# Kernel tuning notes

Hardware: AMD Instinct MI355X
Metric: run time of the kernel (lower is better)

The kernel has to match this reference:

```python
import jax, jax.numpy as jnp
import numpy as np

N_HEAD, D_MODEL, D_HEAD = 16, 1024, 64
QLEN, BSZ = 1024, 8
LN_EPS = 1e-5


def _rel_shift(x):
    # x: [b, n, i, j]; Transformer-XL relative shift via pad/reshape/slice
    b, n, i, j = x.shape
    x = jnp.pad(x, ((0, 0), (0, 0), (0, 0), (1, 0)))  # [b,n,i,j+1]
    x = x.reshape(b, n, j + 1, i)[:, :, 1:, :].reshape(b, n, i, j)
    return x


def setup_inputs() -> dict:
    key = jax.random.key(0)
    k = jax.random.split(key, 8)
    w = jax.random.normal(k[0], (QLEN, BSZ, D_MODEL), dtype=jnp.float32)
    r_emb = jax.random.normal(k[1], (QLEN, N_HEAD, D_HEAD), dtype=jnp.float32) * 0.02
    r_w_bias = jax.random.normal(k[2], (N_HEAD, D_HEAD), dtype=jnp.float32) * 0.02
    r_bias = jax.random.normal(k[3], (QLEN, N_HEAD), dtype=jnp.float32) * 0.02
    # causal mask: True means masked (j > i)
    attn_mask = jnp.triu(jnp.ones((QLEN, QLEN), dtype=bool), k=1)
    qkv_w = jax.random.normal(k[4], (D_MODEL, 3 * N_HEAD * D_HEAD), dtype=jnp.float32) * (D_MODEL ** -0.5)
    o_w = jax.random.normal(k[5], (N_HEAD * D_HEAD, D_MODEL), dtype=jnp.float32) * ((N_HEAD * D_HEAD) ** -0.5)
    ln_g = jnp.ones((D_MODEL,), dtype=jnp.float32)
    ln_b = jnp.zeros((D_MODEL,), dtype=jnp.float32)
    return {"w": w, "r_emb": r_emb, "r_w_bias": r_w_bias, "r_bias": r_bias,
            "qkv_w": qkv_w, "o_w": o_w, "ln_g": ln_g, "ln_b": ln_b,
            "attn_mask": attn_mask}


def reference(w, r_emb, r_w_bias, r_bias, qkv_w, o_w, ln_g, ln_b, attn_mask):
    qlen, bsz, d_model = w.shape
    n_head, d_head = r_w_bias.shape
    scale = 1.0 / (d_head ** 0.5)

    heads = w @ qkv_w  # [q, b, 3*H*D]
    q_h, k_h, v_h = jnp.split(heads, 3, axis=-1)
    q_h = q_h.reshape(qlen, bsz, n_head, d_head)
    k_h = k_h.reshape(qlen, bsz, n_head, d_head)
    v_h = v_h.reshape(qlen, bsz, n_head, d_head)

    # klen == qlen (no mems), r_emb/r_bias already length klen
    rw_q = q_h + r_w_bias[None, None]                      # [i,b,n,d]
    AC = jnp.einsum('ibnd,jbnd->bnij', rw_q, k_h)          # content score
    B_ = jnp.einsum('ibnd,jnd->bnij', q_h, r_emb)          # position score
    D_ = r_bias.T[None, :, None, :]                        # [1,n,1,j]
    BD = _rel_shift(B_ + D_)
    attn_score = scale * (AC + BD)                         # [b,n,i,j]

    attn_score = jnp.where(attn_mask[None, None], -jnp.inf, attn_score)
    attn_prob = jax.nn.softmax(attn_score, axis=3)

    attn_vec = jnp.einsum('bnij,jbnd->ibnd', attn_prob, v_h)
    attn_vec = attn_vec.reshape(qlen, bsz, n_head * d_head)
    attn_out = attn_vec @ o_w

    # post-LN residual
    y = w + attn_out
    mu = jnp.mean(y, axis=-1, keepdims=True)
    var = jnp.mean((y - mu) ** 2, axis=-1, keepdims=True)
    out = (y - mu) * jax.lax.rsqrt(var + LN_EPS) * ln_g + ln_b
    return out
```

## Files before the change

### kernel.cpp

```cpp
#include <hip/hip_runtime.h>

typedef unsigned short u16;
typedef __attribute__((ext_vector_type(8))) short bf16x8;
typedef __attribute__((ext_vector_type(4))) short bf16x4;
typedef __attribute__((ext_vector_type(4))) float f32x4;
typedef __attribute__((ext_vector_type(4))) unsigned short u16x4;

#define SEQ 1024
#define BSZ 8
#define NHD 16
#define DHD 64
#define DMODEL 1024

__device__ __forceinline__ u16 f2bf(float x) {
  unsigned u = __float_as_uint(x);
  return (u16)((u + 0x7fffu + ((u >> 16) & 1u)) >> 16);
}
__device__ __forceinline__ float bf2f(u16 h) {
  return __uint_as_float(((unsigned)h) << 16);
}

typedef const __attribute__((address_space(1))) unsigned int gu32_t;
typedef __attribute__((address_space(3))) unsigned int lu32_t;
__device__ __forceinline__ void gload16(const void* g, void* l) {
  __builtin_amdgcn_global_load_lds((gu32_t*)g, (lu32_t*)l, 16, 0, 0);
}

__global__ void cast_w_k(const float* __restrict__ in, u16* __restrict__ out) {
  size_t i = ((size_t)blockIdx.x * 256 + threadIdx.x) * 4;
  float4 v = *(const float4*)(in + i);
  u16x4 o;
  o[0] = f2bf(v.x); o[1] = f2bf(v.y); o[2] = f2bf(v.z); o[3] = f2bf(v.w);
  *(u16x4*)(out + i) = o;
}

__global__ void transpose_cast_k(const float* __restrict__ in, u16* __restrict__ out,
                                 int R, int C) {
  __shared__ float tile[32][33];
  int tx = threadIdx.x & 31, ty = threadIdx.x >> 5;
  int bx = blockIdx.x * 32, by = blockIdx.y * 32;
#pragma unroll
  for (int rr = ty; rr < 32; rr += 8)
    tile[rr][tx] = in[(size_t)(by + rr) * C + bx + tx];
  __syncthreads();
#pragma unroll
  for (int rr = ty; rr < 32; rr += 8)
    out[(size_t)(bx + rr) * R + by + tx] = f2bf(tile[tx][rr]);
}

__global__ void cast_remb_k(const float* __restrict__ in, u16* __restrict__ out) {
  int t0 = blockIdx.x * 256 + threadIdx.x;
  int jn = t0 >> 3, db = t0 & 7;
  int j = jn >> 4, n = jn & 15;
  const float* src = in + (size_t)jn * 64 + db * 8;
  u16* dst = out + (size_t)n * 65536 + (size_t)(j >> 4) * 1024 + (db >> 2) * 512 +
             (((j & 15) | ((db & 3) << 4)) << 3);
#pragma unroll
  for (int e = 0; e < 8; ++e) dst[e] = f2bf(src[e]);
}

__global__ void cvec_k(const float* __restrict__ remb, const float* __restrict__ rwb,
                       float* __restrict__ cv) {
  int idx = blockIdx.x * 256 + threadIdx.x;
  int n = idx >> 10, t = idx & 1023;
  const float* src = remb + (size_t)(t * 16 + n) * 64;
  const float* wb = rwb + n * 64;
  float s = 0.f;
#pragma unroll
  for (int d = 0; d < 64; ++d) s += src[d] * wb[d];
  cv[idx] = s;
}

template <int EPI>
__global__ __launch_bounds__(256) void gemm_bt(
    const u16* __restrict__ A, const u16* __restrict__ Bt, int K,
    u16* __restrict__ q_o, u16* __restrict__ k_o, u16* __restrict__ v_o,
    const float* __restrict__ resid, float* __restrict__ yout) {
  __shared__ __attribute__((aligned(16))) u16 ldsA[2][4096];
  __shared__ __attribute__((aligned(16))) u16 ldsB[2][4096];
  const int tid = threadIdx.x;
  const int wid = tid >> 6, l = tid & 63;
  const int l15 = l & 15, lg = l >> 4;
  const int bm = blockIdx.y, bn = blockIdx.x;
  const int wm = wid & 1, wn = wid >> 1;
  const size_t ldb = (size_t)K * 2;

  const char* aA = (const char*)A + (size_t)(bm * 128 + wid * 32 + (l >> 2)) * ldb + (l & 3) * 16;
  const char* aB = (const char*)Bt + (size_t)(bn * 128 + wid * 32 + (l >> 2)) * ldb + (l & 3) * 16;

  auto stage = [&](int buf, int kt) {
    const char* sa = aA + (size_t)kt * 64;
    const char* sb = aB + (size_t)kt * 64;
    char* la = (char*)&ldsA[buf][wid * 1024];
    char* lb = (char*)&ldsB[buf][wid * 1024];
    gload16(sa, la);
    gload16(sa + 16 * ldb, la + 1024);
    gload16(sb, lb);
    gload16(sb + 16 * ldb, lb + 1024);
  };

  f32x4 acc[4][4] = {};
  stage(0, 0);
  __syncthreads();
  const int NT = K >> 5;
  for (int t = 0; t < NT; ++t) {
    int cur = t & 1;
    if (t + 1 < NT) stage(cur ^ 1, t + 1);
    bf16x8 af[4], bfr[4];
#pragma unroll
    for (int mi = 0; mi < 4; ++mi)
      af[mi] = *(const bf16x8*)&ldsA[cur][(wm * 64 + mi * 16 + l15) * 32 + lg * 8];
#pragma unroll
    for (int ni = 0; ni < 4; ++ni)
      bfr[ni] = *(const bf16x8*)&ldsB[cur][(wn * 64 + ni * 16 + l15) * 32 + lg * 8];
#pragma unroll
    for (int mi = 0; mi < 4; ++mi)
#pragma unroll
      for (int ni = 0; ni < 4; ++ni)
        acc[mi][ni] = __builtin_amdgcn_mfma_f32_16x16x32_bf16(af[mi], bfr[ni], acc[mi][ni], 0, 0, 0);
    __syncthreads();
  }

  if (EPI == 0) {
#pragma unroll
    for (int mi = 0; mi < 4; ++mi)
#pragma unroll
      for (int ni = 0; ni < 4; ++ni) {
        int c = bn * 128 + wn * 64 + ni * 16 + l15;
        int which = c >> 10, rem = c & 1023, h = rem >> 6, d = rem & 63;
        u16* dst = which == 0 ? q_o : (which == 1 ? k_o : v_o);
#pragma unroll
        for (int r = 0; r < 4; ++r) {
          int rg = bm * 128 + wm * 64 + mi * 16 + lg * 4 + r;
          int i = rg >> 3, bb = rg & 7;
          int bn2 = bb * 16 + h;
          size_t idx;
          if (which == 0) {
            idx = ((size_t)bn2 * 1024 + i) * 64 + d;
          } else if (which == 1) {
            idx = (size_t)bn2 * 65536 + (size_t)(i >> 4) * 1024 + (d >> 5) * 512 +
                  (((i & 15) | (((d >> 3) & 3) << 4)) << 3) + (d & 7);
          } else {
            idx = (size_t)bn2 * 65536 + (size_t)(i >> 4) * 1024 + (d >> 4) * 256 +
                  (((d & 15) | (((i >> 2) & 3) << 4)) << 2) + (i & 3);
          }
          dst[idx] = f2bf(acc[mi][ni][r]);
        }
      }
  } else {
#pragma unroll
    for (int mi = 0; mi < 4; ++mi)
#pragma unroll
      for (int ni = 0; ni < 4; ++ni) {
        int c = bn * 128 + wn * 64 + ni * 16 + l15;
#pragma unroll
        for (int r = 0; r < 4; ++r) {
          int rg = bm * 128 + wm * 64 + mi * 16 + lg * 4 + r;
          size_t off = (size_t)rg * 1024 + c;
          yout[off] = resid[off] + acc[mi][ni][r];
        }
      }
  }
}

__global__ __launch_bounds__(256, 4) void attn_k(
    const u16* __restrict__ qg, const u16* __restrict__ kf, const u16* __restrict__ vf,
    const u16* __restrict__ rf, const float* __restrict__ rbias,
    const float* __restrict__ cvec, const float* __restrict__ rwb,
    u16* __restrict__ av) {
  __shared__ __attribute__((aligned(16))) float Elds[4][16][84];
  __shared__ __attribute__((aligned(16))) float rb[1088];

  const int tid = threadIdx.x;
  const int wid = tid >> 6, l = tid & 63;
  const int l15 = l & 15, lg = l >> 4;
  const int id = blockIdx.x;
  const int qblk = 15 - (id >> 7);
  const int n = (id & 7) | (((id >> 3) & 1) << 3);
  const int b = (id >> 4) & 7;
  const int bn = b * 16 + n;
  const int ib = qblk * 64;
  const int iw = ib + wid * 16;

  for (int idx = tid; idx < 1088; idx += 256)
    rb[idx] = (idx < 1024) ? (rbias[idx * 16 + n] - cvec[n * 1024 + idx]) : 0.f;

  const u16* qrow = qg + ((size_t)bn * 1024 + iw + l15) * 64;
  const float* wbp = rwb + n * 64;
  bf16x8 qr0 = *(const bf16x8*)(qrow + lg * 8);
  bf16x8 qr1 = *(const bf16x8*)(qrow + 32 + lg * 8);
  bf16x8 qw0, qw1;
#pragma unroll
  for (int e = 0; e < 8; ++e) {
    qw0[e] = (short)f2bf(bf2f((u16)qr0[e]) + wbp[lg * 8 + e]);
    qw1[e] = (short)f2bf(bf2f((u16)qr1[e]) + wbp[32 + lg * 8 + e]);
  }

  f32x4 oacc[4] = {};
  float m_run = -1e30f, l_run = 0.f;

  const u16* kfp = kf + (size_t)bn * 65536 + l * 8;
  const u16* vfp = vf + (size_t)bn * 65536 + l * 4;
  const u16* rfp = rf + (size_t)n * 65536 + l * 8;

  __syncthreads();

  const int njt = qblk + 1;
  for (int jt = 0; jt < njt; ++jt) {
    const int jb = jt * 64;

    const u16* kt = kfp + jt * 4096;
    bf16x8 kf00 = *(const bf16x8*)(kt);
    bf16x8 kf01 = *(const bf16x8*)(kt + 512);
    bf16x8 kf10 = *(const bf16x8*)(kt + 1024);
    bf16x8 kf11 = *(const bf16x8*)(kt + 1536);
    bf16x8 kf20 = *(const bf16x8*)(kt + 2048);
    bf16x8 kf21 = *(const bf16x8*)(kt + 2560);
    bf16x8 kf30 = *(const bf16x8*)(kt + 3072);
    bf16x8 kf31 = *(const bf16x8*)(kt + 3584);

    const int tb = jb - iw + 1008;
    const int tb16 = tb >> 4;
#pragma unroll
    for (int f = 0; f < 5; ++f) {
      int t16 = tb16 + f;
      if (t16 > 63) t16 = 63;
      const u16* rr = rfp + t16 * 1024;
      bf16x8 ra0 = *(const bf16x8*)(rr);
      bf16x8 ra1 = *(const bf16x8*)(rr + 512);
      f32x4 et = {};
      et = __builtin_amdgcn_mfma_f32_16x16x32_bf16(ra0, qw0, et, 0, 0, 0);
      et = __builtin_amdgcn_mfma_f32_16x16x32_bf16(ra1, qw1, et, 0, 0, 0);
      f32x4 rb4 = *(const f32x4*)&rb[tb + f * 16 + lg * 4];
      et = et + rb4;
      *(f32x4*)&Elds[wid][l15][f * 16 + lg * 4] = et;
    }

    f32x4 st[4];
    __builtin_amdgcn_s_setprio(1);
    {
      f32x4 a;
      a = __builtin_amdgcn_mfma_f32_16x16x32_bf16(kf00, qw0, (f32x4){}, 0, 0, 0);
      st[0] = __builtin_amdgcn_mfma_f32_16x16x32_bf16(kf01, qw1, a, 0, 0, 0);
      a = __builtin_amdgcn_mfma_f32_16x16x32_bf16(kf10, qw0, (f32x4){}, 0, 0, 0);
      st[1] = __builtin_amdgcn_mfma_f32_16x16x32_bf16(kf11, qw1, a, 0, 0, 0);
      a = __builtin_amdgcn_mfma_f32_16x16x32_bf16(kf20, qw0, (f32x4){}, 0, 0, 0);
      st[2] = __builtin_amdgcn_mfma_f32_16x16x32_bf16(kf21, qw1, a, 0, 0, 0);
      a = __builtin_amdgcn_mfma_f32_16x16x32_bf16(kf30, qw0, (f32x4){}, 0, 0, 0);
      st[3] = __builtin_amdgcn_mfma_f32_16x16x32_bf16(kf31, qw1, a, 0, 0, 0);
    }
    __builtin_amdgcn_s_setprio(0);

    const u16* vt0 = vfp + jt * 4096;
    bf16x4 va0 = *(const bf16x4*)(vt0);
    bf16x4 va1 = *(const bf16x4*)(vt0 + 1024);
    bf16x4 va2 = *(const bf16x4*)(vt0 + 2048);
    bf16x4 va3 = *(const bf16x4*)(vt0 + 3072);

    const bool domask = (jb == ib);
    float tmax = -1e30f;
#pragma unroll
    for (int jj = 0; jj < 4; ++jj)
#pragma unroll
      for (int r2 = 0; r2 < 4; ++r2) {
        int jl = jj * 16 + lg * 4 + r2;
        float v = st[jj][r2] + Elds[wid][l15][jl - l15 + 15];
        v *= 0.125f;
        if (domask && (jl > wid * 16 + l15)) v = -1e30f;
        st[jj][r2] = v;
        tmax = fmaxf(tmax, v);
      }
    tmax = fmaxf(tmax, __shfl_xor(tmax, 16));
    tmax = fmaxf(tmax, __shfl_xor(tmax, 32));

    if (!__all(tmax - m_run <= 8.0f)) {
      float m_new = fmaxf(m_run, tmax);
      float fac = __expf(m_run - m_new);
      m_run = m_new;
      l_run *= fac;
      float fo[4];
#pragma unroll
      for (int r2 = 0; r2 < 4; ++r2) fo[r2] = __shfl(fac, (l & 48) | (lg * 4 + r2));
#pragma unroll
      for (int dd = 0; dd < 4; ++dd)
#pragma unroll
        for (int r2 = 0; r2 < 4; ++r2) oacc[dd][r2] *= fo[r2];
    }

    float psum = 0.f;
    bf16x4 pa[4];
#pragma unroll
    for (int jj = 0; jj < 4; ++jj)
#pragma unroll
      for (int r2 = 0; r2 < 4; ++r2) {
        float p = __expf(st[jj][r2] - m_run);
        psum += p;
        pa[jj][r2] = (short)f2bf(p);
      }
    psum += __shfl_xor(psum, 16);
    psum += __shfl_xor(psum, 32);
    l_run += psum;

    __builtin_amdgcn_s_setprio(1);
    {
      const u16* vt1 = vt0 + 256;
      bf16x4 vb0 = *(const bf16x4*)(vt1);
      bf16x4 vb1 = *(const bf16x4*)(vt1 + 1024);
      bf16x4 vb2 = *(const bf16x4*)(vt1 + 2048);
      bf16x4 vb3 = *(const bf16x4*)(vt1 + 3072);
      oacc[0] = __builtin_amdgcn_mfma_f32_16x16x16bf16_1k(pa[0], va0, oacc[0], 0, 0, 0);
      oacc[0] = __builtin_amdgcn_mfma_f32_16x16x16bf16_1k(pa[1], va1, oacc[0], 0, 0, 0);
      oacc[0] = __builtin_amdgcn_mfma_f32_16x16x16bf16_1k(pa[2], va2, oacc[0], 0, 0, 0);
      oacc[0] = __builtin_amdgcn_mfma_f32_16x16x16bf16_1k(pa[3], va3, oacc[0], 0, 0, 0);
      const u16* vt2 = vt0 + 512;
      va0 = *(const bf16x4*)(vt2);
      va1 = *(const bf16x4*)(vt2 + 1024);
      va2 = *(const bf16x4*)(vt2 + 2048);
      va3 = *(const bf16x4*)(vt2 + 3072);
      oacc[1] = __builtin_amdgcn_mfma_f32_16x16x16bf16_1k(pa[0], vb0, oacc[1], 0, 0, 0);
      oacc[1] = __builtin_amdgcn_mfma_f32_16x16x16bf16_1k(pa[1], vb1, oacc[1], 0, 0, 0);
      oacc[1] = __builtin_amdgcn_mfma_f32_16x16x16bf16_1k(pa[2], vb2, oacc[1], 0, 0, 0);
      oacc[1] = __builtin_amdgcn_mfma_f32_16x16x16bf16_1k(pa[3], vb3, oacc[1], 0, 0, 0);
      const u16* vt3 = vt0 + 768;
      vb0 = *(const bf16x4*)(vt3);
      vb1 = *(const bf16x4*)(vt3 + 1024);
      vb2 = *(const bf16x4*)(vt3 + 2048);
      vb3 = *(const bf16x4*)(vt3 + 3072);
      oacc[2] = __builtin_amdgcn_mfma_f32_16x16x16bf16_1k(pa[0], va0, oacc[2], 0, 0, 0);
      oacc[2] = __builtin_amdgcn_mfma_f32_16x16x16bf16_1k(pa[1], va1, oacc[2], 0, 0, 0);
      oacc[2] = __builtin_amdgcn_mfma_f32_16x16x16bf16_1k(pa[2], va2, oacc[2], 0, 0, 0);
      oacc[2] = __builtin_amdgcn_mfma_f32_16x16x16bf16_1k(pa[3], va3, oacc[2], 0, 0, 0);
      oacc[3] = __builtin_amdgcn_mfma_f32_16x16x16bf16_1k(pa[0], vb0, oacc[3], 0, 0, 0);
      oacc[3] = __builtin_amdgcn_mfma_f32_16x16x16bf16_1k(pa[1], vb1, oacc[3], 0, 0, 0);
      oacc[3] = __builtin_amdgcn_mfma_f32_16x16x16bf16_1k(pa[2], vb2, oacc[3], 0, 0, 0);
      oacc[3] = __builtin_amdgcn_mfma_f32_16x16x16bf16_1k(pa[3], vb3, oacc[3], 0, 0, 0);
    }
    __builtin_amdgcn_s_setprio(0);
  }

  float linv = 1.f / l_run;
  float io[4];
#pragma unroll
  for (int r2 = 0; r2 < 4; ++r2) io[r2] = __shfl(linv, (l & 48) | (lg * 4 + r2));
#pragma unroll
  for (int dd = 0; dd < 4; ++dd)
#pragma unroll
    for (int r2 = 0; r2 < 4; ++r2) {
      int ig = iw + lg * 4 + r2;
      av[((size_t)ig * 8 + b) * 1024 + n * 64 + dd * 16 + l15] = f2bf(oacc[dd][r2] * io[r2]);
    }
}

__global__ void ln_k(float* __restrict__ y, const float* __restrict__ g,
                     const float* __restrict__ be) {
  const int row = blockIdx.x, tid = threadIdx.x;
  float* p = y + (size_t)row * 1024;
  float4 v = ((const float4*)p)[tid];
  float s1 = v.x + v.y + v.z + v.w;
  float s2 = v.x * v.x + v.y * v.y + v.z * v.z + v.w * v.w;
#pragma unroll
  for (int mk = 1; mk < 64; mk <<= 1) {
    s1 += __shfl_xor(s1, mk);
    s2 += __shfl_xor(s2, mk);
  }
  __shared__ float as1[4], as2[4];
  if ((tid & 63) == 0) { as1[tid >> 6] = s1; as2[tid >> 6] = s2; }
  __syncthreads();
  s1 = as1[0] + as1[1] + as1[2] + as1[3];
  s2 = as2[0] + as2[1] + as2[2] + as2[3];
  float mu = s1 * (1.f / 1024.f);
  float var = s2 * (1.f / 1024.f) - mu * mu;
  float rs = rsqrtf(var + 1e-5f);
  float4 gg = ((const float4*)g)[tid];
  float4 bb = ((const float4*)be)[tid];
  float4 o;
  o.x = (v.x - mu) * rs * gg.x + bb.x;
  o.y = (v.y - mu) * rs * gg.y + bb.y;
  o.z = (v.z - mu) * rs * gg.z + bb.z;
  o.w = (v.w - mu) * rs * gg.w + bb.w;
  ((float4*)p)[tid] = o;
}

extern "C" void kernel_launch(void* const* d_in, const int* in_sizes, int n_in,
                              void* d_out, int out_size, void* d_ws, size_t ws_size,
                              hipStream_t stream) {
  (void)in_sizes; (void)n_in; (void)out_size; (void)ws_size;
  const float* w      = (const float*)d_in[0];
  const float* r_emb  = (const float*)d_in[1];
  const float* r_wb   = (const float*)d_in[2];
  const float* r_bias = (const float*)d_in[3];
  const float* qkv_w  = (const float*)d_in[4];
  const float* o_w    = (const float*)d_in[5];
  const float* ln_g   = (const float*)d_in[6];
  const float* ln_b   = (const float*)d_in[7];
  float* out = (float*)d_out;
  char* ws = (char*)d_ws;

  u16* w_b    = (u16*)(ws + 0);
  u16* qkvw_t = (u16*)(ws + 16777216);
  u16* ow_t   = (u16*)(ws + 23068672);
  u16* remb_f = (u16*)(ws + 25165824);
  u16* q_b    = (u16*)(ws + 27262976);
  u16* k_f    = (u16*)(ws + 44040192);
  u16* v_f    = (u16*)(ws + 60817408);
  float* cvb  = (float*)(ws + 77594624);
  u16* av_b   = w_b;

  cast_w_k<<<8192, 256, 0, stream>>>(w, w_b);
  transpose_cast_k<<<dim3(96, 32), 256, 0, stream>>>(qkv_w, qkvw_t, 1024, 3072);
  transpose_cast_k<<<dim3(32, 32), 256, 0, stream>>>(o_w, ow_t, 1024, 1024);
  cast_remb_k<<<512, 256, 0, stream>>>(r_emb, remb_f);
  cvec_k<<<64, 256, 0, stream>>>(r_emb, r_wb, cvb);
  gemm_bt<0><<<dim3(24, 64), 256, 0, stream>>>(w_b, qkvw_t, 1024, q_b, k_f, v_f, nullptr, nullptr);
  attn_k<<<dim3(2048), 256, 0, stream>>>(q_b, k_f, v_f, remb_f, r_bias, cvb, r_wb, av_b);
  gemm_bt<1><<<dim3(8, 64), 256, 0, stream>>>(av_b, ow_t, 1024, nullptr, nullptr, nullptr, w, out);
  ln_k<<<8192, 256, 0, stream>>>(out, ln_g, ln_b);
}
```

Baseline: 224.3 us.

## Process two 16-row query tiles per wave to reuse K/V/R fragment loads

Each wave in the attention kernel now handles 32 query rows (two 16-row tiles A and B) instead of 16, so every K, V and relative-embedding fragment loaded from global memory feeds twice as many MFMAs. The positional-score tile computation is shared across both tiles via six R fragments instead of five per tile, and the grid is halved to 1024 blocks with launch bounds lowered to 3 blocks per CU. This cuts redundant global/L2 traffic per unit of work, at the cost of higher register pressure, lower occupancy and coarser causal load balancing, since waves within a block now have different loop trip counts.

```diff
diff --git a/kernel.cpp b/kernel.cpp
--- a/kernel.cpp
+++ b/kernel.cpp
@@ -163,191 +163,202 @@
   }
 }
 
-__global__ __launch_bounds__(256, 4) void attn_k(
+__global__ __launch_bounds__(256, 3) void attn_k(
     const u16* __restrict__ qg, const u16* __restrict__ kf, const u16* __restrict__ vf,
     const u16* __restrict__ rf, const float* __restrict__ rbias,
     const float* __restrict__ cvec, const float* __restrict__ rwb,
     u16* __restrict__ av) {
-  __shared__ __attribute__((aligned(16))) float Elds[4][16][84];
+  __shared__ __attribute__((aligned(16))) float EldsA[4][16][84];
+  __shared__ __attribute__((aligned(16))) float EldsB[4][16][84];
   __shared__ __attribute__((aligned(16))) float rb[1088];
 
   const int tid = threadIdx.x;
   const int wid = tid >> 6, l = tid & 63;
   const int l15 = l & 15, lg = l >> 4;
   const int id = blockIdx.x;
-  const int qblk = 15 - (id >> 7);
+  const int qblk = 7 - (id >> 7);
   const int n = (id & 7) | (((id >> 3) & 1) << 3);
   const int b = (id >> 4) & 7;
   const int bn = b * 16 + n;
-  const int ib = qblk * 64;
-  const int iw = ib + wid * 16;
+  const int ib = qblk * 128;
+  const int iw = ib + wid * 32;
 
   for (int idx = tid; idx < 1088; idx += 256)
     rb[idx] = (idx < 1024) ? (rbias[idx * 16 + n] - cvec[n * 1024 + idx]) : 0.f;
 
-  const u16* qrow = qg + ((size_t)bn * 1024 + iw + l15) * 64;
   const float* wbp = rwb + n * 64;
-  bf16x8 qr0 = *(const bf16x8*)(qrow + lg * 8);
-  bf16x8 qr1 = *(const bf16x8*)(qrow + 32 + lg * 8);
-  bf16x8 qw0, qw1;
+  const u16* qrowA = qg + ((size_t)bn * 1024 + iw + l15) * 64;
+  const u16* qrowB = qrowA + 16 * 64;
+  bf16x8 qa0 = *(const bf16x8*)(qrowA + lg * 8);
+  bf16x8 qa1 = *(const bf16x8*)(qrowA + 32 + lg * 8);
+  bf16x8 qb0 = *(const bf16x8*)(qrowB + lg * 8);
+  bf16x8 qb1 = *(const bf16x8*)(qrowB + 32 + lg * 8);
+  bf16x8 qwA0, qwA1, qwB0, qwB1;
 #pragma unroll
   for (int e = 0; e < 8; ++e) {
-    qw0[e] = (short)f2bf(bf2f((u16)qr0[e]) + wbp[lg * 8 + e]);
-    qw1[e] = (short)f2bf(bf2f((u16)qr1[e]) + wbp[32 + lg * 8 + e]);
-  }
-
-  f32x4 oacc[4] = {};
-  float m_run = -1e30f, l_run = 0.f;
+    float w0 = wbp[lg * 8 + e], w1 = wbp[32 + lg * 8 + e];
+    qwA0[e] = (short)f2bf(bf2f((u16)qa0[e]) + w0);
+    qwA1[e] = (short)f2bf(bf2f((u16)qa1[e]) + w1);
+    qwB0[e] = (short)f2bf(bf2f((u16)qb0[e]) + w0);
+    qwB1[e] = (short)f2bf(bf2f((u16)qb1[e]) + w1);
+  }
+
+  f32x4 oaccA[4] = {}, oaccB[4] = {};
+  float mA = -1e30f, lA = 0.f, mB = -1e30f, lB = 0.f;
 
   const u16* kfp = kf + (size_t)bn * 65536 + l * 8;
   const u16* vfp = vf + (size_t)bn * 65536 + l * 4;
   const u16* rfp = rf + (size_t)n * 65536 + l * 8;
 
+  const int dAm = (iw & 63) + l15;
+  const int dBm = dAm + 16;
+
   __syncthreads();
 
-  const int njt = qblk + 1;
+  const int njt = (iw >> 6) + 1;
   for (int jt = 0; jt < njt; ++jt) {
     const int jb = jt * 64;
 
     const u16* kt = kfp + jt * 4096;
-    bf16x8 kf00 = *(const bf16x8*)(kt);
-    bf16x8 kf01 = *(const bf16x8*)(kt + 512);
-    bf16x8 kf10 = *(const bf16x8*)(kt + 1024);
-    bf16x8 kf11 = *(const bf16x8*)(kt + 1536);
-    bf16x8 kf20 = *(const bf16x8*)(kt + 2048);
-    bf16x8 kf21 = *(const bf16x8*)(kt + 2560);
-    bf16x8 kf30 = *(const bf16x8*)(kt + 3072);
-    bf16x8 kf31 = *(const bf16x8*)(kt + 3584);
-
-    const int tb = jb - iw + 1008;
-    const int tb16 = tb >> 4;
-#pragma unroll
-    for (int f = 0; f < 5; ++f) {
-      int t16 = tb16 + f;
+    bf16x8 kk[8];
+#pragma unroll
+    for (int s = 0; s < 8; ++s) kk[s] = *(const bf16x8*)(kt + s * 512);
+
+    const int tbB = jb - iw - 16 + 1008;
+    const int t16b = tbB >> 4;
+#pragma unroll
+    for (int f = 0; f < 6; ++f) {
+      int t16 = t16b + f;
       if (t16 > 63) t16 = 63;
       const u16* rr = rfp + t16 * 1024;
       bf16x8 ra0 = *(const bf16x8*)(rr);
       bf16x8 ra1 = *(const bf16x8*)(rr + 512);
-      f32x4 et = {};
-      et = __builtin_amdgcn_mfma_f32_16x16x32_bf16(ra0, qw0, et, 0, 0, 0);
-      et = __builtin_amdgcn_mfma_f32_16x16x32_bf16(ra1, qw1, et, 0, 0, 0);
-      f32x4 rb4 = *(const f32x4*)&rb[tb + f * 16 + lg * 4];
-      et = et + rb4;
-      *(f32x4*)&Elds[wid][l15][f * 16 + lg * 4] = et;
+      f32x4 rb4 = *(const f32x4*)&rb[tbB + f * 16 + lg * 4];
+      if (f < 5) {
+        f32x4 et = {};
+        et = __builtin_amdgcn_mfma_f32_16x16x32_bf16(ra0, qwB0, et, 0, 0, 0);
+        et = __builtin_amdgcn_mfma_f32_16x16x32_bf16(ra1, qwB1, et, 0, 0, 0);
+        *(f32x4*)&EldsB[wid][l15][f * 16 + lg * 4] = et + rb4;
+      }
+      if (f >= 1) {
+        f32x4 et = {};
+        et = __builtin_amdgcn_mfma_f32_16x16x32_bf16(ra0, qwA0, et, 0, 0, 0);
+        et = __builtin_amdgcn_mfma_f32_16x16x32_bf16(ra1, qwA1, et, 0, 0, 0);
+        *(f32x4*)&EldsA[wid][l15][(f - 1) * 16 + lg * 4] = et + rb4;
+      }
     }
 
-    f32x4 st[4];
+    f32x4 stA[4], stB[4];
     __builtin_amdgcn_s_setprio(1);
-    {
-      f32x4 a;
-      a = __builtin_amdgcn_mfma_f32_16x16x32_bf16(kf00, qw0, (f32x4){}, 0, 0, 0);
-      st[0] = __builtin_amdgcn_mfma_f32_16x16x32_bf16(kf01, qw1, a, 0, 0, 0);
-      a = __builtin_amdgcn_mfma_f32_16x16x32_bf16(kf10, qw0, (f32x4){}, 0, 0, 0);
-      st[1] = __builtin_amdgcn_mfma_f32_16x16x32_bf16(kf11, qw1, a, 0, 0, 0);
-      a = __builtin_amdgcn_mfma_f32_16x16x32_bf16(kf20, qw0, (f32x4){}, 0, 0, 0);
-      st[2] = __builtin_amdgcn_mfma_f32_16x16x32_bf16(kf21, qw1, a, 0, 0, 0);
-      a = __builtin_amdgcn_mfma_f32_16x16x32_bf16(kf30, qw0, (f32x4){}, 0, 0, 0);
-      st[3] = __builtin_amdgcn_mfma_f32_16x16x32_bf16(kf31, qw1, a, 0, 0, 0);
+#pragma unroll
+    for (int jj = 0; jj < 4; ++jj) {
+      f32x4 a = __builtin_amdgcn_mfma_f32_16x16x32_bf16(kk[jj * 2], qwA0, (f32x4){}, 0, 0, 0);
+      stA[jj] = __builtin_amdgcn_mfma_f32_16x16x32_bf16(kk[jj * 2 + 1], qwA1, a, 0, 0, 0);
+    }
+#pragma unroll
+    for (int jj = 0; jj < 4; ++jj) {
+      f32x4 a = __builtin_amdgcn_mfma_f32_16x16x32_bf16(kk[jj * 2], qwB0, (f32x4){}, 0, 0, 0);
+      stB[jj] = __builtin_amdgcn_mfma_f32_16x16x32_bf16(kk[jj * 2 + 1], qwB1, a, 0, 0, 0);
     }
     __builtin_amdgcn_s_setprio(0);
 
     const u16* vt0 = vfp + jt * 4096;
-    bf16x4 va0 = *(const bf16x4*)(vt0);
-    bf16x4 va1 = *(const bf16x4*)(vt0 + 1024);
-    bf16x4 va2 = *(const bf16x4*)(vt0 + 2048);
-    bf16x4 va3 = *(const bf16x4*)(vt0 + 3072);
-
-    const bool domask = (jb == ib);
-    float tmax = -1e30f;
+    bf16x4 vv[4][4];
+#pragma unroll
+    for (int jj = 0; jj < 4; ++jj)
+#pragma unroll
+      for (int dd = 0; dd < 4; ++dd)
+        vv[jj][dd] = *(const bf16x4*)(vt0 + jj * 1024 + dd * 256);
+
+    const bool domask = (jt == njt - 1);
+    float tmaxA = -1e30f, tmaxB = -1e30f;
 #pragma unroll
     for (int jj = 0; jj < 4; ++jj)
 #pragma unroll
       for (int r2 = 0; r2 < 4; ++r2) {
         int jl = jj * 16 + lg * 4 + r2;
-        float v = st[jj][r2] + Elds[wid][l15][jl - l15 + 15];
-        v *= 0.125f;
-        if (domask && (jl > wid * 16 + l15)) v = -1e30f;
-        st[jj][r2] = v;
-        tmax = fmaxf(tmax, v);
-      }
-    tmax = fmaxf(tmax, __shfl_xor(tmax, 16));
-    tmax = fmaxf(tmax, __shfl_xor(tmax, 32));
-
-    if (!__all(tmax - m_run <= 8.0f)) {
-      float m_new = fmaxf(m_run, tmax);
-      float fac = __expf(m_run - m_new);
-      m_run = m_new;
-      l_run *= fac;
-      float fo[4];
-#pragma unroll
-      for (int r2 = 0; r2 < 4; ++r2) fo[r2] = __shfl(fac, (l & 48) | (lg * 4 + r2));
+        float va = stA[jj][r2] + EldsA[wid][l15][jl - l15 + 15];
+        float vb = stB[jj][r2] + EldsB[wid][l15][jl - l15 + 15];
+        va *= 0.125f; vb *= 0.125f;
+        if (domask) {
+          if (jl > dAm) va = -1e30f;
+          if (jl > dBm) vb = -1e30f;
+        }
+        stA[jj][r2] = va; stB[jj][r2] = vb;
+        tmaxA = fmaxf(tmaxA, va); tmaxB = fmaxf(tmaxB, vb);
+      }
+    tmaxA = fmaxf(tmaxA, __shfl_xor(tmaxA, 16));
+    tmaxA = fmaxf(tmaxA, __shfl_xor(tmaxA, 32));
+    tmaxB = fmaxf(tmaxB, __shfl_xor(tmaxB, 16));
+    tmaxB = fmaxf(tmaxB, __shfl_xor(tmaxB, 32));
+
+    if (!__all(fmaxf(tmaxA - mA, tmaxB - mB) <= 8.0f)) {
+      float mnA = fmaxf(mA, tmaxA), mnB = fmaxf(mB, tmaxB);
+      float facA = __expf(mA - mnA), facB = __expf(mB - mnB);
+      mA = mnA; mB = mnB;
+      lA *= facA; lB *= facB;
+      float foA[4], foB[4];
+#pragma unroll
+      for (int r2 = 0; r2 < 4; ++r2) {
+        foA[r2] = __shfl(facA, (l & 48) | (lg * 4 + r2));
+        foB[r2] = __shfl(facB, (l & 48) | (lg * 4 + r2));
+      }
 #pragma unroll
       for (int dd = 0; dd < 4; ++dd)
 #pragma unroll
-        for (int r2 = 0; r2 < 4; ++r2) oacc[dd][r2] *= fo[r2];
+        for (int r2 = 0; r2 < 4; ++r2) {
+          oaccA[dd][r2] *= foA[r2];
+          oaccB[dd][r2] *= foB[r2];
+        }
     }
 
-    float psum = 0.f;
-    bf16x4 pa[4];
+    float psA = 0.f, psB = 0.f;
+    bf16x4 paA[4], paB[4];
 #pragma unroll
     for (int jj = 0; jj < 4; ++jj)
 #pragma unroll
       for (int r2 = 0; r2 < 4; ++r2) {
-        float p = __expf(st[jj][r2] - m_run);
-        psum += p;
-        pa[jj][r2] = (short)f2bf(p);
-      }
-    psum += __shfl_xor(psum, 16);
-    psum += __shfl_xor(psum, 32);
-    l_run += psum;
+        float pA = __expf(stA[jj][r2] - mA);
+        float pB = __expf(stB[jj][r2] - mB);
+        psA += pA; psB += pB;
+        paA[jj][r2] = (short)f2bf(pA);
+        paB[jj][r2] = (short)f2bf(pB);
+      }
+    psA += __shfl_xor(psA, 16);
+    psA += __shfl_xor(psA, 32);
+    psB += __shfl_xor(psB, 16);
+    psB += __shfl_xor(psB, 32);
+    lA += psA; lB += psB;
 
     __builtin_amdgcn_s_setprio(1);
-    {
-      const u16* vt1 = vt0 + 256;
-      bf16x4 vb0 = *(const bf16x4*)(vt1);
-      bf16x4 vb1 = *(const bf16x4*)(vt1 + 1024);
-      bf16x4 vb2 = *(const bf16x4*)(vt1 + 2048);
-      bf16x4 vb3 = *(const bf16x4*)(vt1 + 3072);
-      oacc[0] = __builtin_amdgcn_mfma_f32_16x16x16bf16_1k(pa[0], va0, oacc[0], 0, 0, 0);
-      oacc[0] = __builtin_amdgcn_mfma_f32_16x16x16bf16_1k(pa[1], va1, oacc[0], 0, 0, 0);
-      oacc[0] = __builtin_amdgcn_mfma_f32_16x16x16bf16_1k(pa[2], va2, oacc[0], 0, 0, 0);
-      oacc[0] = __builtin_amdgcn_mfma_f32_16x16x16bf16_1k(pa[3], va3, oacc[0], 0, 0, 0);
-      const u16* vt2 = vt0 + 512;
-      va0 = *(const bf16x4*)(vt2);
-      va1 = *(const bf16x4*)(vt2 + 1024);
-      va2 = *(const bf16x4*)(vt2 + 2048);
-      va3 = *(const bf16x4*)(vt2 + 3072);
-      oacc[1] = __builtin_amdgcn_mfma_f32_16x16x16bf16_1k(pa[0], vb0, oacc[1], 0, 0, 0);
-      oacc[1] = __builtin_amdgcn_mfma_f32_16x16x16bf16_1k(pa[1], vb1, oacc[1], 0, 0, 0);
-      oacc[1] = __builtin_amdgcn_mfma_f32_16x16x16bf16_1k(pa[2], vb2, oacc[1], 0, 0, 0);
-      oacc[1] = __builtin_amdgcn_mfma_f32_16x16x16bf16_1k(pa[3], vb3, oacc[1], 0, 0, 0);
-      const u16* vt3 = vt0 + 768;
-      vb0 = *(const bf16x4*)(vt3);
-      vb1 = *(const bf16x4*)(vt3 + 1024);
-      vb2 = *(const bf16x4*)(vt3 + 2048);
-      vb3 = *(const bf16x4*)(vt3 + 3072);
-      oacc[2] = __builtin_amdgcn_mfma_f32_16x16x16bf16_1k(pa[0], va0, oacc[2], 0, 0, 0);
-      oacc[2] = __builtin_amdgcn_mfma_f32_16x16x16bf16_1k(pa[1], va1, oacc[2], 0, 0, 0);
-      oacc[2] = __builtin_amdgcn_mfma_f32_16x16x16bf16_1k(pa[2], va2, oacc[2], 0, 0, 0);
-      oacc[2] = __builtin_amdgcn_mfma_f32_16x16x16bf16_1k(pa[3], va3, oacc[2], 0, 0, 0);
-      oacc[3] = __builtin_amdgcn_mfma_f32_16x16x16bf16_1k(pa[0], vb0, oacc[3], 0, 0, 0);
-      oacc[3] = __builtin_amdgcn_mfma_f32_16x16x16bf16_1k(pa[1], vb1, oacc[3], 0, 0, 0);
-      oacc[3] = __builtin_amdgcn_mfma_f32_16x16x16bf16_1k(pa[2], vb2, oacc[3], 0, 0, 0);
-      oacc[3] = __builtin_amdgcn_mfma_f32_16x16x16bf16_1k(pa[3], vb3, oacc[3], 0, 0, 0);
-    }
+#pragma unroll
+    for (int dd = 0; dd < 4; ++dd)
+#pragma unroll
+      for (int jj = 0; jj < 4; ++jj)
+        oaccA[dd] = __builtin_amdgcn_mfma_f32_16x16x16bf16_1k(paA[jj], vv[jj][dd], oaccA[dd], 0, 0, 0);
+#pragma unroll
+    for (int dd = 0; dd < 4; ++dd)
+#pragma unroll
+      for (int jj = 0; jj < 4; ++jj)
+        oaccB[dd] = __builtin_amdgcn_mfma_f32_16x16x16bf16_1k(paB[jj], vv[jj][dd], oaccB[dd], 0, 0, 0);
     __builtin_amdgcn_s_setprio(0);
   }
 
-  float linv = 1.f / l_run;
-  float io[4];
-#pragma unroll
-  for (int r2 = 0; r2 < 4; ++r2) io[r2] = __shfl(linv, (l & 48) | (lg * 4 + r2));
+  float liA = 1.f / lA, liB = 1.f / lB;
+  float ioA[4], ioB[4];
+#pragma unroll
+  for (int r2 = 0; r2 < 4; ++r2) {
+    ioA[r2] = __shfl(liA, (l & 48) | (lg * 4 + r2));
+    ioB[r2] = __shfl(liB, (l & 48) | (lg * 4 + r2));
+  }
 #pragma unroll
   for (int dd = 0; dd < 4; ++dd)
 #pragma unroll
     for (int r2 = 0; r2 < 4; ++r2) {
-      int ig = iw + lg * 4 + r2;
-      av[((size_t)ig * 8 + b) * 1024 + n * 64 + dd * 16 + l15] = f2bf(oacc[dd][r2] * io[r2]);
+      int igA = iw + lg * 4 + r2;
+      av[((size_t)igA * 8 + b) * 1024 + n * 64 + dd * 16 + l15] = f2bf(oaccA[dd][r2] * ioA[r2]);
+      int igB = igA + 16;
+      av[((size_t)igB * 8 + b) * 1024 + n * 64 + dd * 16 + l15] = f2bf(oaccB[dd][r2] * ioB[r2]);
     }
 }
 
@@ -412,7 +423,7 @@
   cast_remb_k<<<512, 256, 0, stream>>>(r_emb, remb_f);
   cvec_k<<<64, 256, 0, stream>>>(r_emb, r_wb, cvb);
   gemm_bt<0><<<dim3(24, 64), 256, 0, stream>>>(w_b, qkvw_t, 1024, q_b, k_f, v_f, nullptr, nullptr);
-  attn_k<<<dim3(2048), 256, 0, stream>>>(q_b, k_f, v_f, remb_f, r_bias, cvb, r_wb, av_b);
+  attn_k<<<dim3(1024), 256, 0, stream>>>(q_b, k_f, v_f, remb_f, r_bias, cvb, r_wb, av_b);
   gemm_bt<1><<<dim3(8, 64), 256, 0, stream>>>(av_b, ow_t, 1024, nullptr, nullptr, nullptr, w, out);
   ln_k<<<8192, 256, 0, stream>>>(out, ln_g, ln_b);
 }
```

Result: faster. 205.9 us (-8.2%).
